# Kernel optimization log

Measured on AMD Instinct MI355X. Metric: run time of the kernel, lower is better.

## Reference

```python
import jax, jax.numpy as jnp
import numpy as np

B, D, N, H = 2, 8, 40, 128
HID = 4 * H  # 512, MLP hidden width


def setup_inputs() -> dict:
    key = jax.random.key(0)
    ks = jax.random.split(key, 12)
    s_in = 1.0 / np.sqrt(2 * H)
    s_hid = 1.0 / np.sqrt(HID)
    return {
        "node_feature": jax.random.normal(ks[0], (B, D, N, H), jnp.float32),
        "pairwise_feature": jax.random.normal(ks[1], (B, D, N, N, H), jnp.float32),
        # first MLP layer weight [2H, HID] split into node half and pairwise half
        "W1n": jax.random.uniform(ks[2], (H, HID), jnp.float32, -s_in, s_in),
        "W1p": jax.random.uniform(ks[3], (H, HID), jnp.float32, -s_in, s_in),
        "b1": jax.random.uniform(ks[4], (HID,), jnp.float32, -s_in, s_in),
        "W2": jax.random.uniform(ks[5], (HID, HID), jnp.float32, -s_hid, s_hid),
        "b2": jax.random.uniform(ks[6], (HID,), jnp.float32, -s_hid, s_hid),
        "W3": jax.random.uniform(ks[7], (HID, 1), jnp.float32, -s_hid, s_hid),
        "b3": jax.random.uniform(ks[8], (1,), jnp.float32, -s_hid, s_hid),
        "scale": jnp.float32(1.0),
        "bias": jnp.float32(0.0),
    }


def reference(node_feature, pairwise_feature, W1n, W1p, b1, W2, b2, W3, b3, scale, bias):
    # max over the dataset axis
    nf = jnp.max(node_feature, axis=-3)        # [B, N, H]
    pf = jnp.max(pairwise_feature, axis=-4)    # [B, N, N, H]
    # First linear on concat([node_expand, pair_expand]) decomposed into two
    # small projections + broadcast add (mathematically identical to
    # Linear(concat) since W1 = [W1n; W1p]).
    hn = nf @ W1n                               # [B, N, HID]
    hp = pf @ W1p                               # [B, N, N, HID]
    h = jax.nn.relu(hn[:, :, None, None, :] + hp[:, None, :, :, :] + b1)  # [B,N,N,N,HID]
    h = jax.nn.relu(h @ W2 + b2)                # [B, N, N, N, HID]
    v = h @ W3 + b3                             # [B, N, N, N, 1]
    return jax.nn.sigmoid(scale * v + bias).squeeze(-1)  # [B, N, N, N]
```

## Files before the change

### kernel.cpp

```cpp
#include <hip/hip_runtime.h>
#include <math.h>

#define BB 2
#define DD 8
#define NN 40
#define HH 128
#define HID 512
#define NJK 1600
#define MROW 64000

typedef __attribute__((ext_vector_type(8))) short short8;
typedef __attribute__((ext_vector_type(4))) float floatx4;

static __device__ __forceinline__ unsigned short f2bf(float x) {
    unsigned int b = __float_as_uint(x);
    b += 0x7fffu + ((b >> 16) & 1u);
    return (unsigned short)(b >> 16);
}

__global__ __launch_bounds__(256) void prep_kernel(
        const float* __restrict__ node, const float* __restrict__ pair,
        const float* __restrict__ W1n, const float* __restrict__ W1p,
        const float* __restrict__ b1, const float* __restrict__ W2,
        float* __restrict__ hp, float* __restrict__ hnb,
        unsigned short* __restrict__ w2f) {
    __shared__ float smem[32 * 513];
    const int bid = blockIdx.x;
    const int t = threadIdx.x;

    if (bid < 400) {
        float (*pf)[HH] = (float (*)[HH])smem;
        const int rowbase = bid * 8;
        #pragma unroll
        for (int e = t; e < 8*HH; e += 256) {
            int r8 = e >> 7, c = e & 127;
            int grow = rowbase + r8;
            int b = grow / NJK, jk = grow - b*NJK;
            float m = -INFINITY;
            #pragma unroll
            for (int d = 0; d < DD; ++d)
                m = fmaxf(m, pair[((size_t)((b*DD + d)*NJK + jk))*HH + c]);
            pf[r8][c] = m;
        }
        __syncthreads();
        const int rg = t >> 7, c4 = (t & 127) * 4;
        float4 acc[4];
        #pragma unroll
        for (int r = 0; r < 4; ++r) acc[r] = make_float4(0.f,0.f,0.f,0.f);
        #pragma unroll 4
        for (int h = 0; h < HH; ++h) {
            float4 wv = *(const float4*)&W1p[h*HID + c4];
            #pragma unroll
            for (int r = 0; r < 4; ++r) {
                float pv = pf[rg*4 + r][h];
                acc[r].x = fmaf(pv, wv.x, acc[r].x);
                acc[r].y = fmaf(pv, wv.y, acc[r].y);
                acc[r].z = fmaf(pv, wv.z, acc[r].z);
                acc[r].w = fmaf(pv, wv.w, acc[r].w);
            }
        }
        #pragma unroll
        for (int r = 0; r < 4; ++r)
            *(float4*)&hp[(size_t)(rowbase + rg*4 + r)*HID + c4] = acc[r];
    } else if (bid < 410) {
        float (*nf)[HH] = (float (*)[HH])smem;
        const int rowbase = (bid - 400) * 8;
        #pragma unroll
        for (int e = t; e < 8*HH; e += 256) {
            int r8 = e >> 7, c = e & 127;
            int grow = rowbase + r8;
            int b = grow / NN, i = grow - b*NN;
            float m = -INFINITY;
            #pragma unroll
            for (int d = 0; d < DD; ++d)
                m = fmaxf(m, node[((size_t)((b*DD + d)*NN + i))*HH + c]);
            nf[r8][c] = m;
        }
        __syncthreads();
        const int rg = t >> 7, c4 = (t & 127) * 4;
        float4 acc[4];
        #pragma unroll
        for (int r = 0; r < 4; ++r) acc[r] = make_float4(0.f,0.f,0.f,0.f);
        #pragma unroll 4
        for (int h = 0; h < HH; ++h) {
            float4 wv = *(const float4*)&W1n[h*HID + c4];
            #pragma unroll
            for (int r = 0; r < 4; ++r) {
                float nv = nf[rg*4 + r][h];
                acc[r].x = fmaf(nv, wv.x, acc[r].x);
                acc[r].y = fmaf(nv, wv.y, acc[r].y);
                acc[r].z = fmaf(nv, wv.z, acc[r].z);
                acc[r].w = fmaf(nv, wv.w, acc[r].w);
            }
        }
        float4 b1v = *(const float4*)&b1[c4];
        #pragma unroll
        for (int r = 0; r < 4; ++r) {
            float4 o = make_float4(acc[r].x + b1v.x, acc[r].y + b1v.y,
                                   acc[r].z + b1v.z, acc[r].w + b1v.w);
            *(float4*)&hnb[(size_t)(rowbase + rg*4 + r)*HID + c4] = o;
        }
    } else {
        const int ks = bid - 410;
        for (int e = t; e < 32*HID; e += 256) {
            int r = e >> 9, c = e & 511;
            smem[r*513 + c] = W2[(size_t)(ks*32 + r)*HID + c];
        }
        __syncthreads();
        const int w = t >> 6, l = t & 63;
        const int lr = l & 15, lg = l >> 4;
        #pragma unroll
        for (int f = 0; f < 8; ++f) {
            int cf = w*8 + f;
            short8 u;
            #pragma unroll
            for (int kk = 0; kk < 8; ++kk)
                u[kk] = (short)f2bf(smem[(lg*8 + kk)*513 + cf*16 + lr]);
            *(short8*)(w2f + (size_t)(cf*16 + ks)*512 + l*8) = u;
        }
    }
}

__global__ __launch_bounds__(512, 4) void main_kernel(
        const float* __restrict__ hp, const float* __restrict__ hnb,
        const unsigned short* __restrict__ w2f,
        const float* __restrict__ b2, const float* __restrict__ W3,
        const float* __restrict__ b3, const float* __restrict__ scale,
        const float* __restrict__ bias, float* __restrict__ out) {
    __shared__ __align__(16) unsigned short h1s[64 * HID];
    __shared__ float red[8][64];

    const int bid  = blockIdx.x;
    const int bid8 = (bid & 7)*250 + (bid >> 3);
    const int b    = bid8 / 1000;
    const int rem  = bid8 % 1000;
    const int i0   = (rem / 100) * 4;
    const int jk0  = (rem % 100) * 16;
    const int t    = threadIdx.x;
    char* h1c = (char*)h1s;

    const int w  = t >> 6, l = t & 63;
    const int lr = l & 15, lg = l >> 4;

    const unsigned short* bbase = w2f + (size_t)w*32768 + l*8;
    short8 bcur[4];
    #pragma unroll
    for (int tn = 0; tn < 4; ++tn)
        bcur[tn] = *(const short8*)(bbase + ((tn*16) << 9));

    {
        const float* hrow = hp + ((size_t)(b*NJK + jk0 + lr))*HID;
        const float* nbase = hnb + ((size_t)(b*NN + i0))*HID;
        #pragma unroll
        for (int j = 0; j < 8; ++j) {
            int ks = w*2 + (j >> 2), mi = j & 3;
            int k0 = ks*32 + lg*8;
            const float* hr = hrow + k0;
            const float* nr = nbase + mi*HID + k0;
            float4 p0 = *(const float4*)hr, p1 = *(const float4*)(hr + 4);
            float4 n0 = *(const float4*)nr, n1 = *(const float4*)(nr + 4);
            short8 u;
            u[0] = (short)f2bf(fmaxf(p0.x + n0.x, 0.f));
            u[1] = (short)f2bf(fmaxf(p0.y + n0.y, 0.f));
            u[2] = (short)f2bf(fmaxf(p0.z + n0.z, 0.f));
            u[3] = (short)f2bf(fmaxf(p0.w + n0.w, 0.f));
            u[4] = (short)f2bf(fmaxf(p1.x + n1.x, 0.f));
            u[5] = (short)f2bf(fmaxf(p1.y + n1.y, 0.f));
            u[6] = (short)f2bf(fmaxf(p1.z + n1.z, 0.f));
            u[7] = (short)f2bf(fmaxf(p1.w + n1.w, 0.f));
            *(short8*)(h1c + ((ks*4 + mi) << 10) + l*16) = u;
        }
    }
    __syncthreads();

    floatx4 acc[4][4];
    #pragma unroll
    for (int mi = 0; mi < 4; ++mi)
        #pragma unroll
        for (int tn = 0; tn < 4; ++tn)
            acc[mi][tn] = (floatx4){0.f, 0.f, 0.f, 0.f};

    #pragma unroll 1
    for (int ks = 0; ks < 16; ++ks) {
        short8 bnxt[4];
        int ksn = (ks + 1) & 15;
        #pragma unroll
        for (int tn = 0; tn < 4; ++tn)
            bnxt[tn] = *(const short8*)(bbase + ((tn*16 + ksn) << 9));
        short8 av[4];
        #pragma unroll
        for (int mi = 0; mi < 4; ++mi)
            av[mi] = *(const short8*)(h1c + ((ks*4 + mi) << 10) + l*16);
        __builtin_amdgcn_s_setprio(1);
        #pragma unroll
        for (int mi = 0; mi < 4; ++mi)
            #pragma unroll
            for (int tn = 0; tn < 4; ++tn)
                acc[mi][tn] = __builtin_amdgcn_mfma_f32_16x16x32_bf16(av[mi], bcur[tn], acc[mi][tn], 0, 0, 0);
        __builtin_amdgcn_s_setprio(0);
        #pragma unroll
        for (int tn = 0; tn < 4; ++tn) bcur[tn] = bnxt[tn];
    }

    float b2v[4], w3v[4];
    #pragma unroll
    for (int tn = 0; tn < 4; ++tn) {
        int col = w*64 + tn*16 + lr;
        b2v[tn] = b2[col];
        w3v[tn] = W3[col];
    }
    #pragma unroll
    for (int mi = 0; mi < 4; ++mi) {
        #pragma unroll
        for (int q = 0; q < 4; ++q) {
            float s = 0.f;
            #pragma unroll
            for (int tn = 0; tn < 4; ++tn)
                s += fmaxf(acc[mi][tn][q] + b2v[tn], 0.f) * w3v[tn];
            s += __shfl_xor(s, 1);
            s += __shfl_xor(s, 2);
            s += __shfl_xor(s, 4);
            s += __shfl_xor(s, 8);
            if (lr == 0) red[w][mi*16 + lg*4 + q] = s;
        }
    }
    __syncthreads();
    if (t < 64) {
        float v = b3[0];
        #pragma unroll
        for (int c = 0; c < 8; ++c) v += red[c][t];
        float z = scale[0]*v + bias[0];
        int il = t >> 4, jl = t & 15;
        out[(size_t)b*MROW + (size_t)(i0 + il)*NJK + jk0 + jl] =
            1.0f / (1.0f + expf(-z));
    }
}

extern "C" void kernel_launch(void* const* d_in, const int* in_sizes, int n_in,
                              void* d_out, int out_size, void* d_ws, size_t ws_size,
                              hipStream_t stream) {
    const float* node  = (const float*)d_in[0];
    const float* pair  = (const float*)d_in[1];
    const float* W1n   = (const float*)d_in[2];
    const float* W1p   = (const float*)d_in[3];
    const float* b1    = (const float*)d_in[4];
    const float* W2    = (const float*)d_in[5];
    const float* b2    = (const float*)d_in[6];
    const float* W3    = (const float*)d_in[7];
    const float* b3    = (const float*)d_in[8];
    const float* scale = (const float*)d_in[9];
    const float* bias  = (const float*)d_in[10];
    float* out = (float*)d_out;

    float* hp  = (float*)d_ws;
    float* hnb = hp + (size_t)BB*NJK*HID;
    unsigned short* w2f = (unsigned short*)(hnb + BB*NN*HID);

    hipLaunchKernelGGL(prep_kernel, dim3(426), dim3(256), 0, stream,
                       node, pair, W1n, W1p, b1, W2, hp, hnb, w2f);
    hipLaunchKernelGGL(main_kernel, dim3(2000), dim3(512), 0, stream,
                       hp, hnb, w2f, b2, W3, b3, scale, bias, out);
}
```

Baseline: 181.0 us.

## Make main kernel persistent with double-buffered LDS tile staging

The main kernel now launches 250 blocks, each processing 8 consecutive 64x512 tiles instead of one tile per block. The next tile's h1 activations are loaded from global memory, combined, and written into a second LDS buffer while the MFMA loop works on the current one. The per-block setup (b2/W3 loads) is amortized across tiles. This trades occupancy (launch bounds 512,2 and 128KB of shared memory) and leaves only 250 blocks, which may underfill the GPU's compute units, for overlap of the global loads with the matrix math.

```diff
diff --git a/kernel.cpp b/kernel.cpp
--- a/kernel.cpp
+++ b/kernel.cpp
@@ -1,4 +1,5 @@
 #include <hip/hip_runtime.h>
+#include <hip/hip_bf16.h>
 #include <math.h>
 
 #define BB 2
@@ -17,6 +18,17 @@
     b += 0x7fffu + ((b >> 16) & 1u);
     return (unsigned short)(b >> 16);
 }
+
+static __device__ __forceinline__ short bfr(float x) {
+    x = fmaxf(x, 0.f);
+    __hip_bfloat16 h = __float2bfloat16(x);
+    return (short)__builtin_bit_cast(unsigned short, h);
+}
+
+#define COORD(tau, b_, i0_, jk0_) do { \
+    int _b = (tau)/1000; int _rem = (tau) - _b*1000; \
+    int _ig = _rem/100;  int _jc = _rem - _ig*100; \
+    b_ = _b; i0_ = _ig*4; jk0_ = _jc*16; } while (0)
 
 __global__ __launch_bounds__(256) void prep_kernel(
         const float* __restrict__ node, const float* __restrict__ pair,
@@ -121,118 +133,154 @@
     }
 }
 
-__global__ __launch_bounds__(512, 4) void main_kernel(
+__global__ __launch_bounds__(512, 2) void main_kernel(
         const float* __restrict__ hp, const float* __restrict__ hnb,
         const unsigned short* __restrict__ w2f,
         const float* __restrict__ b2, const float* __restrict__ W3,
         const float* __restrict__ b3, const float* __restrict__ scale,
         const float* __restrict__ bias, float* __restrict__ out) {
-    __shared__ __align__(16) unsigned short h1s[64 * HID];
+    __shared__ __align__(16) unsigned short h1d[2 * 32768];
     __shared__ float red[8][64];
 
-    const int bid  = blockIdx.x;
-    const int bid8 = (bid & 7)*250 + (bid >> 3);
-    const int b    = bid8 / 1000;
-    const int rem  = bid8 % 1000;
-    const int i0   = (rem / 100) * 4;
-    const int jk0  = (rem % 100) * 16;
-    const int t    = threadIdx.x;
-    char* h1c = (char*)h1s;
-
-    const int w  = t >> 6, l = t & 63;
+    const int bid = blockIdx.x;
+    const int xq = bid & 7, xi = bid >> 3;
+    const int sb = (xq < 2) ? xq*32 + xi : 64 + (xq - 2)*31 + xi;
+    const int t = threadIdx.x;
+    const int ww = t >> 6, l = t & 63;
     const int lr = l & 15, lg = l >> 4;
-
-    const unsigned short* bbase = w2f + (size_t)w*32768 + l*8;
+    char* h1c = (char*)h1d;
+
+    const unsigned short* bbase = w2f + (size_t)ww*32768 + l*8;
+
+    float b2v[4], w3v[4];
+    #pragma unroll
+    for (int tn = 0; tn < 4; ++tn) {
+        int col = ww*64 + tn*16 + lr;
+        b2v[tn] = b2[col];
+        w3v[tn] = W3[col];
+    }
+
+    {
+        int b0, i00, jk00;
+        COORD(sb*8, b0, i00, jk00);
+        #pragma unroll
+        for (int j = 0; j < 8; ++j) {
+            const int ksf = ww*2 + (j >> 2), smi = j & 3;
+            const float* hr = hp  + ((size_t)(b0*NJK + jk00 + lr))*HID + ksf*32 + lg*8;
+            const float* nr = hnb + ((size_t)(b0*NN  + i00 + smi))*HID + ksf*32 + lg*8;
+            float4 p0 = *(const float4*)hr, p1 = *(const float4*)(hr + 4);
+            float4 n0 = *(const float4*)nr, n1 = *(const float4*)(nr + 4);
+            short8 u;
+            u[0] = bfr(p0.x + n0.x); u[1] = bfr(p0.y + n0.y);
+            u[2] = bfr(p0.z + n0.z); u[3] = bfr(p0.w + n0.w);
+            u[4] = bfr(p1.x + n1.x); u[5] = bfr(p1.y + n1.y);
+            u[6] = bfr(p1.z + n1.z); u[7] = bfr(p1.w + n1.w);
+            *(short8*)(h1c + ((ksf*4 + smi) << 10) + l*16) = u;
+        }
+    }
+    __syncthreads();
+
     short8 bcur[4];
     #pragma unroll
     for (int tn = 0; tn < 4; ++tn)
         bcur[tn] = *(const short8*)(bbase + ((tn*16) << 9));
 
-    {
-        const float* hrow = hp + ((size_t)(b*NJK + jk0 + lr))*HID;
-        const float* nbase = hnb + ((size_t)(b*NN + i0))*HID;
-        #pragma unroll
-        for (int j = 0; j < 8; ++j) {
-            int ks = w*2 + (j >> 2), mi = j & 3;
-            int k0 = ks*32 + lg*8;
-            const float* hr = hrow + k0;
-            const float* nr = nbase + mi*HID + k0;
-            float4 p0 = *(const float4*)hr, p1 = *(const float4*)(hr + 4);
-            float4 n0 = *(const float4*)nr, n1 = *(const float4*)(nr + 4);
-            short8 u;
-            u[0] = (short)f2bf(fmaxf(p0.x + n0.x, 0.f));
-            u[1] = (short)f2bf(fmaxf(p0.y + n0.y, 0.f));
-            u[2] = (short)f2bf(fmaxf(p0.z + n0.z, 0.f));
-            u[3] = (short)f2bf(fmaxf(p0.w + n0.w, 0.f));
-            u[4] = (short)f2bf(fmaxf(p1.x + n1.x, 0.f));
-            u[5] = (short)f2bf(fmaxf(p1.y + n1.y, 0.f));
-            u[6] = (short)f2bf(fmaxf(p1.z + n1.z, 0.f));
-            u[7] = (short)f2bf(fmaxf(p1.w + n1.w, 0.f));
-            *(short8*)(h1c + ((ks*4 + mi) << 10) + l*16) = u;
-        }
-    }
-    __syncthreads();
-
-    floatx4 acc[4][4];
-    #pragma unroll
-    for (int mi = 0; mi < 4; ++mi)
-        #pragma unroll
-        for (int tn = 0; tn < 4; ++tn)
-            acc[mi][tn] = (floatx4){0.f, 0.f, 0.f, 0.f};
-
-    #pragma unroll 1
-    for (int ks = 0; ks < 16; ++ks) {
-        short8 bnxt[4];
-        int ksn = (ks + 1) & 15;
-        #pragma unroll
-        for (int tn = 0; tn < 4; ++tn)
-            bnxt[tn] = *(const short8*)(bbase + ((tn*16 + ksn) << 9));
-        short8 av[4];
+    for (int tt = 0; tt < 8; ++tt) {
+        const int tau = sb*8 + tt;
+        int b, i0, jk0;   COORD(tau, b, i0, jk0);
+        int bn, i0n, jk0n; COORD(tau + 1, bn, i0n, jk0n);
+        const int cur = tt & 1;
+        char* bufc = h1c + cur*65536;
+        char* bufn = h1c + (cur ^ 1)*65536;
+        const bool st = (tt < 7);
+
+        floatx4 acc[4][4];
         #pragma unroll
         for (int mi = 0; mi < 4; ++mi)
-            av[mi] = *(const short8*)(h1c + ((ks*4 + mi) << 10) + l*16);
-        __builtin_amdgcn_s_setprio(1);
+            #pragma unroll
+            for (int tn = 0; tn < 4; ++tn)
+                acc[mi][tn] = (floatx4){0.f, 0.f, 0.f, 0.f};
+
+        short8 acur[4], anxt[4];
         #pragma unroll
         for (int mi = 0; mi < 4; ++mi)
+            acur[mi] = *(const short8*)(bufc + (mi << 10) + l*16);
+
+        float4 sp0, sp1, sn0, sn1;
+
+        #pragma unroll
+        for (int ks = 0; ks < 16; ++ks) {
+            short8 bnxt[4];
+            const int ksn = (ks + 1) & 15;
             #pragma unroll
             for (int tn = 0; tn < 4; ++tn)
-                acc[mi][tn] = __builtin_amdgcn_mfma_f32_16x16x32_bf16(av[mi], bcur[tn], acc[mi][tn], 0, 0, 0);
-        __builtin_amdgcn_s_setprio(0);
-        #pragma unroll
-        for (int tn = 0; tn < 4; ++tn) bcur[tn] = bnxt[tn];
-    }
-
-    float b2v[4], w3v[4];
-    #pragma unroll
-    for (int tn = 0; tn < 4; ++tn) {
-        int col = w*64 + tn*16 + lr;
-        b2v[tn] = b2[col];
-        w3v[tn] = W3[col];
-    }
-    #pragma unroll
-    for (int mi = 0; mi < 4; ++mi) {
-        #pragma unroll
-        for (int q = 0; q < 4; ++q) {
-            float s = 0.f;
-            #pragma unroll
-            for (int tn = 0; tn < 4; ++tn)
-                s += fmaxf(acc[mi][tn][q] + b2v[tn], 0.f) * w3v[tn];
-            s += __shfl_xor(s, 1);
-            s += __shfl_xor(s, 2);
-            s += __shfl_xor(s, 4);
-            s += __shfl_xor(s, 8);
-            if (lr == 0) red[w][mi*16 + lg*4 + q] = s;
-        }
-    }
-    __syncthreads();
-    if (t < 64) {
-        float v = b3[0];
-        #pragma unroll
-        for (int c = 0; c < 8; ++c) v += red[c][t];
-        float z = scale[0]*v + bias[0];
-        int il = t >> 4, jl = t & 15;
-        out[(size_t)b*MROW + (size_t)(i0 + il)*NJK + jk0 + jl] =
-            1.0f / (1.0f + expf(-z));
+                bnxt[tn] = *(const short8*)(bbase + ((tn*16 + ksn) << 9));
+            if (ks < 15) {
+                #pragma unroll
+                for (int mi = 0; mi < 4; ++mi)
+                    anxt[mi] = *(const short8*)(bufc + (((ks+1)*4 + mi) << 10) + l*16);
+            }
+            if ((ks & 1) == 0) {
+                if (st) {
+                    const int j = ks >> 1;
+                    const int ksf = ww*2 + (j >> 2), smi = j & 3;
+                    const float* hr = hp  + ((size_t)(bn*NJK + jk0n + lr))*HID + ksf*32 + lg*8;
+                    const float* nr = hnb + ((size_t)(bn*NN  + i0n + smi))*HID + ksf*32 + lg*8;
+                    sp0 = *(const float4*)hr; sp1 = *(const float4*)(hr + 4);
+                    sn0 = *(const float4*)nr; sn1 = *(const float4*)(nr + 4);
+                }
+            } else {
+                if (st) {
+                    const int j = ks >> 1;
+                    const int ksf = ww*2 + (j >> 2), smi = j & 3;
+                    short8 u;
+                    u[0] = bfr(sp0.x + sn0.x); u[1] = bfr(sp0.y + sn0.y);
+                    u[2] = bfr(sp0.z + sn0.z); u[3] = bfr(sp0.w + sn0.w);
+                    u[4] = bfr(sp1.x + sn1.x); u[5] = bfr(sp1.y + sn1.y);
+                    u[6] = bfr(sp1.z + sn1.z); u[7] = bfr(sp1.w + sn1.w);
+                    *(short8*)(bufn + ((ksf*4 + smi) << 10) + l*16) = u;
+                }
+            }
+            __builtin_amdgcn_s_setprio(1);
+            #pragma unroll
+            for (int mi = 0; mi < 4; ++mi)
+                #pragma unroll
+                for (int tn = 0; tn < 4; ++tn)
+                    acc[mi][tn] = __builtin_amdgcn_mfma_f32_16x16x32_bf16(acur[mi], bcur[tn], acc[mi][tn], 0, 0, 0);
+            __builtin_amdgcn_s_setprio(0);
+            #pragma unroll
+            for (int tn = 0; tn < 4; ++tn) bcur[tn] = bnxt[tn];
+            if (ks < 15) {
+                #pragma unroll
+                for (int mi = 0; mi < 4; ++mi) acur[mi] = anxt[mi];
+            }
+        }
+        __syncthreads();
+
+        #pragma unroll
+        for (int mi = 0; mi < 4; ++mi) {
+            #pragma unroll
+            for (int q = 0; q < 4; ++q) {
+                float s = 0.f;
+                #pragma unroll
+                for (int tn = 0; tn < 4; ++tn)
+                    s += fmaxf(acc[mi][tn][q] + b2v[tn], 0.f) * w3v[tn];
+                s += __shfl_xor(s, 1);
+                s += __shfl_xor(s, 2);
+                s += __shfl_xor(s, 4);
+                s += __shfl_xor(s, 8);
+                if (lr == 0) red[ww][mi*16 + lg*4 + q] = s;
+            }
+        }
+        __syncthreads();
+        if (t < 64) {
+            float v = b3[0];
+            #pragma unroll
+            for (int c = 0; c < 8; ++c) v += red[c][t];
+            float z = scale[0]*v + bias[0];
+            out[(size_t)b*MROW + (size_t)(i0 + (t >> 4))*NJK + jk0 + (t & 15)] =
+                1.0f / (1.0f + expf(-z));
+        }
     }
 }
 
@@ -258,6 +306,6 @@
 
     hipLaunchKernelGGL(prep_kernel, dim3(426), dim3(256), 0, stream,
                        node, pair, W1n, W1p, b1, W2, hp, hnb, w2f);
-    hipLaunchKernelGGL(main_kernel, dim3(2000), dim3(512), 0, stream,
+    hipLaunchKernelGGL(main_kernel, dim3(250), dim3(512), 0, stream,
                        hp, hnb, w2f, b2, W3, b3, scale, bias, out);
 }
```

New measurement: 269.0 us. 1.49x slower.
